# Kernel tuning notes

Measured on AMD Instinct MI355X. Metric: run time of the kernel, lower is better.

Reference implementation:

```python
import jax, jax.numpy as jnp
import numpy as np


def setup_inputs() -> dict:
    key = jax.random.key(0)
    k1, k2, k3 = jax.random.split(key, 3)
    B, S, D, V, C = 32, 2048, 512, 32000, 2
    tokens = jax.random.randint(k1, (B, S), 0, V, dtype=jnp.int64)
    emb_table = jax.random.normal(k2, (V, D), dtype=jnp.float32) * 0.02
    cls_w = jax.random.normal(k3, (C, D), dtype=jnp.float32) * 0.02
    cls_b = jnp.zeros((C,), dtype=jnp.float32)
    return {"tokens": tokens, "emb_table": emb_table, "cls_w": cls_w, "cls_b": cls_b}


def reference(tokens, emb_table, cls_w, cls_b):
    # Embedding lookup: [B,S,D]
    x = emb_table[tokens]
    # Unscaled self-attention (no 1/sqrt(d), no mask applied, as in source)
    scores = jnp.einsum('bsd,btd->bst', x, x)       # [B,S,S]
    attn = jax.nn.softmax(scores, axis=-1)
    out = jnp.einsum('bst,btd->bsd', attn, x)       # [B,S,D]
    # pool_type == 'select': take first token
    pooled = out[:, 0, :]                            # [B,D]
    logits = pooled @ cls_w.T + cls_b                # [B,C]
    return logits
```

## Files before the change

kernel.cpp:

```cpp
#include <hip/hip_runtime.h>
#include <math.h>

#define BB 32
#define SS 2048
#define DD 512
#define TPW 8
#define WAVES 4
#define TPB (WAVES * TPW)
#define NCHUNK (SS / TPB)

__global__ __launch_bounds__(256) void attn_cls_pass1(
    const int* __restrict__ tokens, const float* __restrict__ emb,
    const float* __restrict__ cls_w, float4* __restrict__ part)
{
    const int b     = blockIdx.x;
    const int chunk = blockIdx.y;
    const int tid   = threadIdx.x;
    const int wave  = tid >> 6;
    const int lane  = tid & 63;

    const int qtok = tokens[(size_t)b * SS];
    const float4* q4 = (const float4*)(emb + (size_t)qtok * DD);
    const float4 qa = q4[lane * 2];
    const float4 qb = q4[lane * 2 + 1];

    const float4* w4 = (const float4*)cls_w;
    const float4 w0a = w4[lane * 2],            w0b = w4[lane * 2 + 1];
    const float4 w1a = w4[(DD/4) + lane * 2],   w1b = w4[(DD/4) + lane * 2 + 1];

    const int tbase = chunk * TPB + wave * TPW;
    int mytok = 0;
    if (lane < TPW) mytok = tokens[(size_t)b * SS + tbase + lane];

    float L = 0.f, d0 = 0.f, d1 = 0.f;

    const int t0 = __shfl(mytok, 0);
    const int t1 = __shfl(mytok, 1);
    const float4* r4 = (const float4*)(emb + (size_t)t0 * DD);
    float4 pa0 = r4[lane * 2], pb0 = r4[lane * 2 + 1];
    r4 = (const float4*)(emb + (size_t)t1 * DD);
    float4 pa1 = r4[lane * 2], pb1 = r4[lane * 2 + 1];

#pragma unroll
    for (int i = 0; i < TPW; ++i) {
        const float4 ra = pa0, rb = pb0;
        pa0 = pa1; pb0 = pb1;
        if (i + 2 < TPW) {
            const int nt = __shfl(mytok, i + 2);
            r4 = (const float4*)(emb + (size_t)nt * DD);
            pa1 = r4[lane * 2]; pb1 = r4[lane * 2 + 1];
        }

        float s = qa.x*ra.x + qa.y*ra.y + qa.z*ra.z + qa.w*ra.w
                + qb.x*rb.x + qb.y*rb.y + qb.z*rb.z + qb.w*rb.w;
#pragma unroll
        for (int off = 32; off > 0; off >>= 1)
            s += __shfl_xor(s, off);

        const float p = __expf(s);
        L += p;
        d0 += p * (w0a.x*ra.x + w0a.y*ra.y + w0a.z*ra.z + w0a.w*ra.w
                 + w0b.x*rb.x + w0b.y*rb.y + w0b.z*rb.z + w0b.w*rb.w);
        d1 += p * (w1a.x*ra.x + w1a.y*ra.y + w1a.z*ra.z + w1a.w*ra.w
                 + w1b.x*rb.x + w1b.y*rb.y + w1b.z*rb.z + w1b.w*rb.w);
    }

#pragma unroll
    for (int off = 32; off > 0; off >>= 1) {
        d0 += __shfl_xor(d0, off);
        d1 += __shfl_xor(d1, off);
    }

    __shared__ float sL[WAVES], s0[WAVES], s1[WAVES];
    if (lane == 0) { sL[wave] = L; s0[wave] = d0; s1[wave] = d1; }
    __syncthreads();
    if (tid == 0) {
        const float Lt = sL[0] + sL[1] + sL[2] + sL[3];
        const float a0 = s0[0] + s0[1] + s0[2] + s0[3];
        const float a1 = s1[0] + s1[1] + s1[2] + s1[3];
        part[(size_t)b * NCHUNK + chunk] = make_float4(Lt, a0, a1, 0.f);
    }
}

__global__ __launch_bounds__(64) void cls_merge(
    const float4* __restrict__ part, const float* __restrict__ cls_b,
    float* __restrict__ out)
{
    const int b    = blockIdx.x;
    const int lane = threadIdx.x;

    const float4 v = part[(size_t)b * NCHUNK + lane];
    float L = v.x, d0 = v.y, d1 = v.z;
#pragma unroll
    for (int off = 32; off > 0; off >>= 1) {
        L  += __shfl_xor(L,  off);
        d0 += __shfl_xor(d0, off);
        d1 += __shfl_xor(d1, off);
    }
    if (lane == 0) {
        const float inv = 1.0f / L;
        out[b * 2 + 0] = d0 * inv + cls_b[0];
        out[b * 2 + 1] = d1 * inv + cls_b[1];
    }
}

extern "C" void kernel_launch(void* const* d_in, const int* in_sizes, int n_in,
                              void* d_out, int out_size, void* d_ws, size_t ws_size,
                              hipStream_t stream)
{
    const int*   tokens = (const int*)  d_in[0];
    const float* emb    = (const float*)d_in[1];
    const float* cls_w  = (const float*)d_in[2];
    const float* cls_b  = (const float*)d_in[3];
    float*       out    = (float*)d_out;

    float4* part = (float4*)d_ws;

    dim3 g1(BB, NCHUNK);
    attn_cls_pass1<<<g1, 256, 0, stream>>>(tokens, emb, cls_w, part);
    cls_merge<<<BB, 64, 0, stream>>>(part, cls_b, out);
}
```

Before: 107.3 us.

## Precompute query and classifier scores over the whole vocabulary, then gather per token

```diff
diff --git a/kernel.cpp b/kernel.cpp
--- a/kernel.cpp
+++ b/kernel.cpp
@@ -4,103 +4,176 @@
 #define BB 32
 #define SS 2048
 #define DD 512
-#define TPW 8
-#define WAVES 4
-#define TPB (WAVES * TPW)
-#define NCHUNK (SS / TPB)
+#define VV 32000
+#define JT 36
+#define RB 256
+#define DH 256
+#define NT 8
 
-__global__ __launch_bounds__(256) void attn_cls_pass1(
+__global__ __launch_bounds__(128) void build_qt(
     const int* __restrict__ tokens, const float* __restrict__ emb,
-    const float* __restrict__ cls_w, float4* __restrict__ part)
+    const float* __restrict__ cls_w, float* __restrict__ QT)
 {
-    const int b     = blockIdx.x;
-    const int chunk = blockIdx.y;
-    const int tid   = threadIdx.x;
-    const int wave  = tid >> 6;
-    const int lane  = tid & 63;
+    const int j   = blockIdx.x;
+    const int tid = threadIdx.x;
+    float4 v = make_float4(0.f, 0.f, 0.f, 0.f);
+    if (j < 32) {
+        const int tok = tokens[(size_t)j * SS];
+        v = ((const float4*)(emb + (size_t)tok * DD))[tid];
+    } else if (j < 34) {
+        v = ((const float4*)(cls_w + (size_t)(j - 32) * DD))[tid];
+    }
+    ((float4*)QT)[j * (DD / 4) + tid] = v;
+}
 
-    const int qtok = tokens[(size_t)b * SS];
-    const float4* q4 = (const float4*)(emb + (size_t)qtok * DD);
-    const float4 qa = q4[lane * 2];
-    const float4 qb = q4[lane * 2 + 1];
+__global__ __launch_bounds__(256) void score_pass(
+    const float* __restrict__ emb, const float* __restrict__ QT,
+    float* __restrict__ Sh)
+{
+    const int bx   = blockIdx.x;
+    const int h    = blockIdx.y;
+    const int tid  = threadIdx.x;
+    const int rowg = tid >> 2;
+    const int jg   = tid & 3;
 
-    const float4* w4 = (const float4*)cls_w;
-    const float4 w0a = w4[lane * 2],            w0b = w4[lane * 2 + 1];
-    const float4 w1a = w4[(DD/4) + lane * 2],   w1b = w4[(DD/4) + lane * 2 + 1];
+    __shared__ float rt[RB][36];
+    __shared__ float qt[JT][36];
 
-    const int tbase = chunk * TPB + wave * TPW;
-    int mytok = 0;
-    if (lane < TPW) mytok = tokens[(size_t)b * SS + tbase + lane];
+    const int v0     = bx * RB;
+    const int dbase4 = (h * DH) >> 2;
+
+    float acc[4][9];
+#pragma unroll
+    for (int k = 0; k < 4; ++k)
+#pragma unroll
+        for (int jj = 0; jj < 9; ++jj) acc[k][jj] = 0.f;
+
+    const float4* emb4 = (const float4*)emb;
+    const float4* QT4  = (const float4*)QT;
+
+    float4 pr[8];
+    float4 pq[2];
+
+    {
+        const int t4 = dbase4;
+#pragma unroll
+        for (int u = 0; u < 8; ++u) {
+            const int f = u * 256 + tid, r = f >> 3, dq = f & 7;
+            pr[u] = emb4[(size_t)(v0 + r) * (DD / 4) + t4 + dq];
+        }
+#pragma unroll
+        for (int u = 0; u < 2; ++u) {
+            const int f = u * 256 + tid;
+            if (f < JT * 8) {
+                const int j = f >> 3, dq = f & 7;
+                pq[u] = QT4[j * (DD / 4) + t4 + dq];
+            }
+        }
+    }
+
+    for (int tt = 0; tt < NT; ++tt) {
+#pragma unroll
+        for (int u = 0; u < 8; ++u) {
+            const int f = u * 256 + tid, r = f >> 3, dq = f & 7;
+            *(float4*)&rt[r][dq * 4] = pr[u];
+        }
+#pragma unroll
+        for (int u = 0; u < 2; ++u) {
+            const int f = u * 256 + tid;
+            if (f < JT * 8) {
+                const int j = f >> 3, dq = f & 7;
+                *(float4*)&qt[j][dq * 4] = pq[u];
+            }
+        }
+        __syncthreads();
+
+        if (tt + 1 < NT) {
+            const int t4 = dbase4 + (tt + 1) * 8;
+#pragma unroll
+            for (int u = 0; u < 8; ++u) {
+                const int f = u * 256 + tid, r = f >> 3, dq = f & 7;
+                pr[u] = emb4[(size_t)(v0 + r) * (DD / 4) + t4 + dq];
+            }
+#pragma unroll
+            for (int u = 0; u < 2; ++u) {
+                const int f = u * 256 + tid;
+                if (f < JT * 8) {
+                    const int j = f >> 3, dq = f & 7;
+                    pq[u] = QT4[j * (DD / 4) + t4 + dq];
+                }
+            }
+        }
+
+#pragma unroll
+        for (int c = 0; c < 8; ++c) {
+            float4 x[4];
+#pragma unroll
+            for (int k = 0; k < 4; ++k)
+                x[k] = *(const float4*)&rt[rowg + 64 * k][c * 4];
+            float4 qv[9];
+#pragma unroll
+            for (int jj = 0; jj < 9; ++jj)
+                qv[jj] = *(const float4*)&qt[jg * 9 + jj][c * 4];
+#pragma unroll
+            for (int k = 0; k < 4; ++k)
+#pragma unroll
+                for (int jj = 0; jj < 9; ++jj)
+                    acc[k][jj] += x[k].x * qv[jj].x + x[k].y * qv[jj].y
+                                + x[k].z * qv[jj].z + x[k].w * qv[jj].w;
+        }
+        __syncthreads();
+    }
+
+    float* outp = Sh + (size_t)h * VV * JT;
+#pragma unroll
+    for (int k = 0; k < 4; ++k) {
+        float* dst = outp + (size_t)(v0 + rowg + 64 * k) * JT + jg * 9;
+#pragma unroll
+        for (int jj = 0; jj < 9; ++jj) dst[jj] = acc[k][jj];
+    }
+}
+
+__global__ __launch_bounds__(256) void gather_pass(
+    const int* __restrict__ tokens, const float* __restrict__ Sh,
+    const float* __restrict__ cls_b, float* __restrict__ out)
+{
+    const int b   = blockIdx.x;
+    const int tid = threadIdx.x;
+    const float* S0 = Sh;
+    const float* S1 = Sh + (size_t)VV * JT;
 
     float L = 0.f, d0 = 0.f, d1 = 0.f;
-
-    const int t0 = __shfl(mytok, 0);
-    const int t1 = __shfl(mytok, 1);
-    const float4* r4 = (const float4*)(emb + (size_t)t0 * DD);
-    float4 pa0 = r4[lane * 2], pb0 = r4[lane * 2 + 1];
-    r4 = (const float4*)(emb + (size_t)t1 * DD);
-    float4 pa1 = r4[lane * 2], pb1 = r4[lane * 2 + 1];
-
 #pragma unroll
-    for (int i = 0; i < TPW; ++i) {
-        const float4 ra = pa0, rb = pb0;
-        pa0 = pa1; pb0 = pb1;
-        if (i + 2 < TPW) {
-            const int nt = __shfl(mytok, i + 2);
-            r4 = (const float4*)(emb + (size_t)nt * DD);
-            pa1 = r4[lane * 2]; pb1 = r4[lane * 2 + 1];
-        }
-
-        float s = qa.x*ra.x + qa.y*ra.y + qa.z*ra.z + qa.w*ra.w
-                + qb.x*rb.x + qb.y*rb.y + qb.z*rb.z + qb.w*rb.w;
-#pragma unroll
-        for (int off = 32; off > 0; off >>= 1)
-            s += __shfl_xor(s, off);
-
+    for (int i = 0; i < 8; ++i) {
+        const int t   = tid * 8 + i;
+        const int tok = tokens[(size_t)b * SS + t];
+        const float* r0 = S0 + (size_t)tok * JT;
+        const float* r1 = S1 + (size_t)tok * JT;
+        const float s = r0[b]  + r1[b];
+        const float u = r0[32] + r1[32];
+        const float v = r0[33] + r1[33];
         const float p = __expf(s);
-        L += p;
-        d0 += p * (w0a.x*ra.x + w0a.y*ra.y + w0a.z*ra.z + w0a.w*ra.w
-                 + w0b.x*rb.x + w0b.y*rb.y + w0b.z*rb.z + w0b.w*rb.w);
-        d1 += p * (w1a.x*ra.x + w1a.y*ra.y + w1a.z*ra.z + w1a.w*ra.w
-                 + w1b.x*rb.x + w1b.y*rb.y + w1b.z*rb.z + w1b.w*rb.w);
+        L += p; d0 += p * u; d1 += p * v;
     }
 
 #pragma unroll
     for (int off = 32; off > 0; off >>= 1) {
+        L  += __shfl_xor(L,  off);
         d0 += __shfl_xor(d0, off);
         d1 += __shfl_xor(d1, off);
     }
 
-    __shared__ float sL[WAVES], s0[WAVES], s1[WAVES];
+    __shared__ float sL[4], s0[4], s1[4];
+    const int wave = tid >> 6, lane = tid & 63;
     if (lane == 0) { sL[wave] = L; s0[wave] = d0; s1[wave] = d1; }
     __syncthreads();
     if (tid == 0) {
         const float Lt = sL[0] + sL[1] + sL[2] + sL[3];
         const float a0 = s0[0] + s0[1] + s0[2] + s0[3];
         const float a1 = s1[0] + s1[1] + s1[2] + s1[3];
-        part[(size_t)b * NCHUNK + chunk] = make_float4(Lt, a0, a1, 0.f);
-    }
-}
-
-__global__ __launch_bounds__(64) void cls_merge(
-    const float4* __restrict__ part, const float* __restrict__ cls_b,
-    float* __restrict__ out)
-{
-    const int b    = blockIdx.x;
-    const int lane = threadIdx.x;
-
-    const float4 v = part[(size_t)b * NCHUNK + lane];
-    float L = v.x, d0 = v.y, d1 = v.z;
-#pragma unroll
-    for (int off = 32; off > 0; off >>= 1) {
-        L  += __shfl_xor(L,  off);
-        d0 += __shfl_xor(d0, off);
-        d1 += __shfl_xor(d1, off);
-    }
-    if (lane == 0) {
-        const float inv = 1.0f / L;
-        out[b * 2 + 0] = d0 * inv + cls_b[0];
-        out[b * 2 + 1] = d1 * inv + cls_b[1];
+        const float inv = 1.0f / Lt;
+        out[b * 2 + 0] = a0 * inv + cls_b[0];
+        out[b * 2 + 1] = a1 * inv + cls_b[1];
     }
 }
 
@@ -114,9 +187,10 @@
     const float* cls_b  = (const float*)d_in[3];
     float*       out    = (float*)d_out;
 
-    float4* part = (float4*)d_ws;
+    float* QT = (float*)d_ws;
+    float* Sh = QT + (size_t)JT * DD;
 
-    dim3 g1(BB, NCHUNK);
-    attn_cls_pass1<<<g1, 256, 0, stream>>>(tokens, emb, cls_w, part);
-    cls_merge<<<BB, 64, 0, stream>>>(part, cls_b, out);
+    build_qt<<<JT, 128, 0, stream>>>(tokens, emb, cls_w, QT);
+    score_pass<<<dim3(125, 2), 256, 0, stream>>>(emb, QT, Sh);
+    gather_pass<<<BB, 256, 0, stream>>>(tokens, Sh, cls_b, out);
 }
```

Result: slower. 182.8 us (+70.3%).
